# Kernel optimization log

Measured on AMD Instinct MI355X. Metric: run time of the kernel, lower is better.

Reference implementation:

```python
import jax, jax.numpy as jnp
import numpy as np

K = 3            # CRF kernel size
THETA0 = 0.5     # color bandwidth
THETA1 = 30.0    # spatial bandwidth
ALPHA0 = 3.0     # kernel scale
BASE = 0.45      # label clamping base
CRF_ITERS = 10   # mean-field iterations
NMS_SIGMA = 2.0  # gaussian matrix-NMS sigma


def _unfold(x, k=K):
    # torch.nn.Unfold(k, stride=1, padding=k//2): (B, C, H, W) -> (B, C, k*k, H*W)
    B, C, H, W = x.shape
    p = k // 2
    xp = jnp.pad(x, ((0, 0), (0, 0), (p, p), (p, p)))
    patches = jnp.stack([xp[:, :, i:i + H, j:j + W]
                         for i in range(k) for j in range(k)], axis=2)
    return patches.reshape(B, C, k * k, H * W)


def _matrix_nms(seg_masks, cate_labels, cate_scores, sigma=NMS_SIGMA):
    n = seg_masks.shape[0]
    m = seg_masks.reshape(n, -1).astype(jnp.float32)
    sum_m = m.sum(axis=1)                         # (n,)
    inter = m @ m.T                               # (n, n)
    union = sum_m[None, :] + sum_m[:, None] - inter
    triu = jnp.triu(jnp.ones((n, n), dtype=bool), k=1)
    iou = jnp.where(triu, inter / union, 0.0)
    label_eq = (cate_labels[None, :] == cate_labels[:, None]) & triu
    decay_iou = jnp.where(label_eq, iou, 0.0)
    comp = decay_iou.max(axis=0)                  # compensate IoU per candidate
    decay = jnp.exp(-sigma * decay_iou ** 2)
    compm = jnp.exp(-sigma * comp ** 2)[:, None]  # broadcast over columns (torch expand+T)
    coef = (decay / compm).min(axis=0)
    return cate_scores * coef


def _crf(feature_map, x, targets):
    B, C, H, W = feature_map.shape
    k2 = K * K
    # gaussian pairwise kernel from (shifted) color features
    fm = feature_map + 10.0
    uf = _unfold(fm)                              # (B, C, k2, H*W)
    idx = np.arange(k2)
    spatial = ((idx // K - K // 2) ** 2 + (idx % K - K // 2) ** 2).astype(np.float32)
    color = -((uf - fm.reshape(B, C, 1, H * W)) ** 2).sum(axis=1) / (2.0 * THETA0 ** 2)
    kernel = ALPHA0 * jnp.exp(color - jnp.asarray(spatial)[None, :, None] / (2.0 * THETA1 ** 2))
    kernel = kernel[:, None]                      # (B, 1, k2, H*W)

    # unary init
    xt = x * targets
    xt = (xt > 0.5).astype(jnp.float32) * (1.0 - 2.0 * BASE) + BASE
    ret = jnp.concatenate([1.0 - xt, xt], axis=1)  # (B, 2, H, W)
    ones_t = jnp.ones_like(targets)
    for _ in range(CRF_ITERS):
        uf_x = _unfold(-jnp.log(ret.reshape(2 * B, 1, H, W))).reshape(B, 2, k2, H * W)
        aggre = (uf_x * kernel).sum(axis=2)        # (B, 2, H*W)
        f = jnp.exp(-aggre).reshape(B, 2, H, W)
        f = f * jnp.concatenate([ones_t, targets], axis=1)  # gate fg channel by targets
        f = f + 1e-6
        f = f / f.sum(axis=1, keepdims=True)
        ret = (f > 0.5).astype(jnp.float32) * (1.0 - 2.0 * BASE) + BASE
    masks = (ret[:, 1:] > 0.5).astype(jnp.float32)  # (B, 1, H, W)
    count = masks.reshape(B, -1).sum(axis=1)
    valid = ((count >= H * W * 0.05) & (count <= H * W * 0.95)).astype(jnp.float32)
    return masks, valid


def setup_inputs() -> dict:
    key = jax.random.key(0)
    k1, k2, k3, k4, k5, k6 = jax.random.split(key, 6)
    n, h, w = 256, 128, 128
    ni, c = 64, 3
    seg_masks = (jax.random.uniform(k1, (n, h, w)) > 0.5).astype(jnp.float32)
    cate_scores = jnp.sort(jax.random.uniform(k2, (n,)))[::-1]
    feature_map = jax.random.uniform(k3, (ni, c, h, w))
    x = jax.random.uniform(k4, (ni, 1, h, w))
    targets = (jax.random.uniform(k5, (ni, 1, h, w)) > 0.3).astype(jnp.float32)
    cate_labels = jax.random.randint(k6, (n,), 0, 80, dtype=jnp.int64)
    return {"seg_masks": seg_masks, "cate_scores": cate_scores,
            "feature_map": feature_map, "x": x, "targets": targets,
            "cate_labels": cate_labels}


def reference(seg_masks, cate_scores, feature_map, x, targets, cate_labels):
    scores = _matrix_nms(seg_masks, cate_labels, cate_scores)
    masks, valid = _crf(feature_map, x, targets)
    return scores, masks, valid
```

## Files before the change

kernel.cpp:

```cpp
#include <hip/hip_runtime.h>
#include <stdint.h>

#define HW 16384
#define NI 64
#define NM 256
#define WORDS 256

#define PR 136
#define PSZ (26 * PR)
#define SR 34

#define OFF_STATE2 (1u << 20)
#define OFF_PACKED (2u << 20)
#define OFF_DIOUT  0x280000u
#define OFF_COMPM  0x2C0000u
#define OFF_CNT    0x2C1000u

__global__ __launch_bounds__(256) void diou_compm_kernel(
    const unsigned long long* __restrict__ packed, const int* __restrict__ labels,
    float* __restrict__ diouT, float* __restrict__ compm) {
    #pragma clang fp contract(off)
    __shared__ unsigned long long colj[WORDS];
    __shared__ float red[NM];
    const int j = blockIdx.x, i = threadIdx.x;
    colj[i] = packed[i * NM + j];
    __syncthreads();
    int inter = 0, si = 0, sj = 0;
    for (int w = 0; w < WORDS; ++w) {
        unsigned long long a = colj[w];
        unsigned long long b = packed[w * NM + i];
        inter += __popcll(a & b);
        sj += __popcll(a);
        si += __popcll(b);
    }
    float d = 0.0f;
    if (j > i && labels[i] == labels[j]) {
        float u = (float)(si + sj - inter);
        d = (float)inter / u;
    }
    diouT[j * NM + i] = d;
    red[i] = d;
    __syncthreads();
    for (int off = 128; off > 0; off >>= 1) {
        if (i < off) red[i] = fmaxf(red[i], red[i + off]);
        __syncthreads();
    }
    if (i == 0) {
        float m = red[0];
        float t = m * m;
        compm[j] = expf(-2.0f * t);
    }
}

template <bool FIRST>
__global__ __launch_bounds__(832, 6) void crf5_kernel(
    const float* __restrict__ feat, const float* __restrict__ scores,
    const float* __restrict__ diouT, const float* __restrict__ compm,
    const float* __restrict__ seg, unsigned long long* __restrict__ packed,
    const float* __restrict__ x, const float* __restrict__ targets,
    unsigned char* __restrict__ state2, float* __restrict__ out,
    int* __restrict__ counters) {
    #pragma clang fp contract(off)
    __shared__ float plane[4 * PSZ];
    __shared__ uint32_t stw[2][26 * SR];
    __shared__ int chg;
    const int tid = threadIdx.x, bid = blockIdx.x;
    const int img = bid >> 3, r0 = (bid & 7) * 16;
    const int w0 = r0 - 5;
    const int rel = tid >> 5;
    const int q = tid & 31;
    const int xc = q * 4;
    const int y = w0 + rel;
    const bool inimg = (unsigned)y < 128u;

    if (FIRST) {
        const int wave = tid >> 6, lane = tid & 63;
        const int gw = bid * 13 + wave;
        if (gw < 4096) {
            for (int t = 0; t < 16; ++t) {
                int gwi = gw * 16 + t;
                int i = gwi >> 8, w = gwi & 255;
                float v = seg[(size_t)i * HW + w * 64 + lane];
                unsigned long long m = __ballot(v > 0.5f);
                if (lane == 0) packed[w * NM + i] = m;
            }
        }
        if (bid == 0 && tid < NI + 1) counters[tid] = 0;
    } else {
        if (bid < NM) {
            float* red = plane;
            if (tid < NM) {
                float d = diouT[bid * NM + tid];
                float dd = d * d;
                float dec = expf(-2.0f * dd);
                red[tid] = dec / compm[tid];
            }
            __syncthreads();
            for (int off = 128; off > 0; off >>= 1) {
                if (tid < off) red[tid] = fminf(red[tid], red[tid + off]);
                __syncthreads();
            }
            if (tid == 0) out[bid] = scores[bid] * red[0];
            __syncthreads();
        }
    }

    {
        const float* fb = feat + (size_t)img * 3 * HW;
        float c0[4], c1[4], c2[4];
        if (inimg) {
            const int pp = y * 128 + xc;
            float4 cv0 = *(const float4*)&fb[pp];
            float4 cv1 = *(const float4*)&fb[HW + pp];
            float4 cv2 = *(const float4*)&fb[2 * HW + pp];
            c0[0]=cv0.x+10.0f; c0[1]=cv0.y+10.0f; c0[2]=cv0.z+10.0f; c0[3]=cv0.w+10.0f;
            c1[0]=cv1.x+10.0f; c1[1]=cv1.y+10.0f; c1[2]=cv1.z+10.0f; c1[3]=cv1.w+10.0f;
            c2[0]=cv2.x+10.0f; c2[1]=cv2.y+10.0f; c2[2]=cv2.z+10.0f; c2[3]=cv2.w+10.0f;
        }
        #pragma unroll
        for (int k = 0; k < 4; ++k) {
            const int dy = (k < 3) ? -1 : 0;
            const int dx = (k < 3) ? (k - 1) : -1;
            float res[4] = {0.0f, 0.0f, 0.0f, 0.0f};
            if (inimg) {
                const int ny = y + dy;
                if ((unsigned)ny < 128u) {
                    #pragma unroll
                    for (int j = 0; j < 4; ++j) {
                        const int nx = xc + j + dx;
                        if ((unsigned)nx < 128u) {
                            const int qq = ny * 128 + nx;
                            float u0 = fb[qq] + 10.0f;
                            float u1 = fb[HW + qq] + 10.0f;
                            float u2 = fb[2 * HW + qq] + 10.0f;
                            float d0 = u0 - c0[j], d1 = u1 - c1[j], d2 = u2 - c2[j];
                            float ss = d0 * d0;
                            ss = ss + d1 * d1;
                            ss = ss + d2 * d2;
                            float color = (-ss) / 0.5f;
                            float sp = (float)(dy * dy + dx * dx) / 1800.0f;
                            res[j] = 3.0f * expf(color - sp);
                        }
                    }
                }
            }
            *(float4*)&plane[k * PSZ + rel * PR + 4 + xc] =
                make_float4(res[0], res[1], res[2], res[3]);
            if (q == 0)
                *(float4*)&plane[k * PSZ + rel * PR + 0] = make_float4(0, 0, 0, 0);
            if (q == 31)
                *(float4*)&plane[k * PSZ + rel * PR + 132] = make_float4(0, 0, 0, 0);
        }
        uint32_t st = 0;
        if (inimg) {
            if (FIRST) {
                const size_t gp = (size_t)img * HW + y * 128 + xc;
                const float4 xv = *(const float4*)(x + gp);
                const float4 tv = *(const float4*)(targets + gp);
                float xs[4] = {xv.x, xv.y, xv.z, xv.w};
                float ts[4] = {tv.x, tv.y, tv.z, tv.w};
                #pragma unroll
                for (int j = 0; j < 4; ++j) {
                    float xt = xs[j] * ts[j];
                    int b1 = (xt > 0.5f) ? 1 : 0;
                    int tb = (ts[j] > 0.5f) ? 1 : 0;
                    st |= (uint32_t)(b1 | ((b1 ^ 1) << 1) | (tb << 2)) << (8 * j);
                }
            } else {
                st = ((const uint32_t*)(state2 + (size_t)img * HW + y * 128))[q];
            }
        }
        stw[0][rel * SR + 1 + q] = st;
        if (!inimg) stw[1][rel * SR + 1 + q] = 0;
        if (q == 0)  { stw[0][rel * SR + 0]  = 0; stw[1][rel * SR + 0]  = 0; }
        if (q == 31) { stw[0][rel * SR + 33] = 0; stw[1][rel * SR + 33] = 0; }
    }
    __syncthreads();

    const float l45 = 0.7985076962177716f;
    const float l55 = 0.5978370007556204f;
    const bool compute = inimg && (y >= r0 - 4) && (y < r0 + 20);
    const int lane = tid & 63;
    const int rbase = rel * PR + 4 + xc;
    const int sbase = rel * SR + 1 + q;
    int cur = 0;
    for (int s = 0; s < 5; ++s) {
        if (tid == 0) chg = 0;
        __syncthreads();
        const int lo = (r0 - 4 + s < 0) ? 0 : r0 - 4 + s;
        const int hi = (r0 + 20 - s > 128) ? 128 : r0 + 20 - s;
        const bool act = compute && (y >= lo) && (y < hi);
        bool changed = false;
        if (act) {
            const uint32_t* sw = &stw[cur][0];
            float lx1r[3][6], lx0r[3][6];
            uint32_t wcen = 0;
            #pragma unroll
            for (int r = 0; r < 3; ++r) {
                const int base = sbase + (r - 1) * SR;
                const uint32_t wm = sw[base - 1];
                const uint32_t wc = sw[base];
                const uint32_t wp = sw[base + 1];
                if (r == 1) wcen = wc;
                unsigned char b[6];
                b[0] = wm >> 24;
                b[1] = wc & 0xff; b[2] = (wc >> 8) & 0xff;
                b[3] = (wc >> 16) & 0xff; b[4] = wc >> 24;
                b[5] = wp & 0xff;
                #pragma unroll
                for (int m = 0; m < 6; ++m) {
                    lx1r[r][m] = (b[m] & 1) ? l55 : l45;
                    lx0r[r][m] = (b[m] & 2) ? l55 : l45;
                }
            }
            float4 p0a = *(const float4*)&plane[0 * PSZ + rbase];
            float4 p1a = *(const float4*)&plane[1 * PSZ + rbase];
            float4 p2a = *(const float4*)&plane[2 * PSZ + rbase];
            float4 p3a = *(const float4*)&plane[3 * PSZ + rbase];
            float4 p0b = *(const float4*)&plane[0 * PSZ + rbase + PR];
            float4 p1b = *(const float4*)&plane[1 * PSZ + rbase + PR];
            float4 p2b = *(const float4*)&plane[2 * PSZ + rbase + PR];
            float s5 = plane[3 * PSZ + rbase + 4];
            float s6 = plane[2 * PSZ + rbase + PR - 1];
            float s8 = plane[0 * PSZ + rbase + PR + 4];
            const float kw[9][4] = {
                {p0a.x, p0a.y, p0a.z, p0a.w},
                {p1a.x, p1a.y, p1a.z, p1a.w},
                {p2a.x, p2a.y, p2a.z, p2a.w},
                {p3a.x, p3a.y, p3a.z, p3a.w},
                {3.0f, 3.0f, 3.0f, 3.0f},
                {p3a.y, p3a.z, p3a.w, s5},
                {s6, p2b.x, p2b.y, p2b.z},
                {p1b.x, p1b.y, p1b.z, p1b.w},
                {p0b.y, p0b.z, p0b.w, s8}};
            float a0[4] = {0.f, 0.f, 0.f, 0.f}, a1[4] = {0.f, 0.f, 0.f, 0.f};
            #pragma unroll
            for (int k = 0; k < 9; ++k) {
                const int r = k / 3, m0 = k % 3;
                #pragma unroll
                for (int j = 0; j < 4; ++j) {
                    const float kwv = kw[k][j];
                    const float t1 = lx1r[r][j + m0] * kwv;
                    const float t0 = lx0r[r][j + m0] * kwv;
                    a1[j] = a1[j] + t1;
                    a0[j] = a0[j] + t0;
                }
            }
            uint32_t ow = 0;
            #pragma unroll
            for (int j = 0; j < 4; ++j) {
                const unsigned char sc = (wcen >> (8 * j)) & 0xffu;
                const float tval = (sc & 4) ? 1.0f : 0.0f;
                const float e1 = expf(-a1[j]);
                const float e0 = expf(-a0[j]);
                const float m1 = e1 * tval;
                const float f1 = m1 + 1e-6f;
                const float f0 = e0 + 1e-6f;
                const float den = f0 + f1;
                const float r1 = f1 / den;
                const float r0v = f0 / den;
                const int s1 = (r1 > 0.5f) ? 1 : 0;
                const int s0 = (r0v > 0.5f) ? 1 : 0;
                ow |= (uint32_t)(s1 | (s0 << 1) | (sc & 4)) << (8 * j);
            }
            stw[cur ^ 1][sbase] = ow;
            changed = (ow != wcen);
        }
        unsigned long long bal = __ballot(changed);
        if (lane == 0 && bal) atomicOr(&chg, 1);
        __syncthreads();
        if (chg == 0) break;
        cur ^= 1;
    }

    int cnt = 0;
    if (inimg && y >= r0 && y < r0 + 16) {
        const uint32_t w = stw[cur][sbase];
        if (FIRST) {
            ((uint32_t*)(state2 + (size_t)img * HW))[y * 32 + q] = w;
        } else {
            float* om = out + NM + (size_t)img * HW;
            *(float4*)(om + y * 128 + xc) =
                make_float4((float)(w & 1), (float)((w >> 8) & 1),
                            (float)((w >> 16) & 1), (float)((w >> 24) & 1));
            cnt = __popc(w & 0x01010101u);
        }
    }

    if (!FIRST) {
        __syncthreads();
        int* cred = (int*)plane;
        cred[tid] = cnt;
        if (tid < 192) cred[832 + tid] = 0;
        __syncthreads();
        for (int off = 512; off > 0; off >>= 1) {
            if (tid < off) cred[tid] += cred[tid + off];
            __syncthreads();
        }
        int* flag = (int*)&stw[0][0];
        if (tid == 0) {
            atomicAdd(&counters[img], cred[0]);
            __threadfence();
            int old = atomicAdd(&counters[NI], 1);
            flag[0] = (old == 511) ? 1 : 0;
        }
        __syncthreads();
        if (flag[0] && tid < NI) {
            int c = atomicAdd(&counters[tid], 0);
            out[NM + (size_t)NI * HW + tid] = (c >= 820 && c <= 15564) ? 1.0f : 0.0f;
        }
    }
}

extern "C" void kernel_launch(void* const* d_in, const int* in_sizes, int n_in,
                              void* d_out, int out_size, void* d_ws, size_t ws_size,
                              hipStream_t stream) {
    const float* seg = (const float*)d_in[0];
    const float* cate_scores = (const float*)d_in[1];
    const float* feat = (const float*)d_in[2];
    const float* x = (const float*)d_in[3];
    const float* targets = (const float*)d_in[4];
    const int* labels = (const int*)d_in[5];
    float* out = (float*)d_out;
    char* ws = (char*)d_ws;

    unsigned char* state2 = (unsigned char*)(ws + OFF_STATE2);
    unsigned long long* packed = (unsigned long long*)(ws + OFF_PACKED);
    float* diouT = (float*)(ws + OFF_DIOUT);
    float* compm = (float*)(ws + OFF_COMPM);
    int* counters = (int*)(ws + OFF_CNT);

    crf5_kernel<true><<<512, 832, 0, stream>>>(feat, cate_scores, diouT, compm,
                                               seg, packed, x, targets, state2,
                                               out, counters);
    diou_compm_kernel<<<NM, 256, 0, stream>>>(packed, labels, diouT, compm);
    crf5_kernel<false><<<512, 832, 0, stream>>>(feat, cate_scores, diouT, compm,
                                                seg, packed, x, targets, state2,
                                                out, counters);
}
```

Baseline: 189.2 us.

## Cache pairwise kernel planes in workspace and skip unchanged CRF stencil updates

The first CRF pass now writes its computed Gaussian pairwise-kernel planes to a global workspace buffer, and the second pass reloads them instead of recomputing them from the feature map. Inside the mean-field loop, each thread remembers its previous 3x3 neighbourhood state words and reuses the prior output when they are unchanged, skipping the weighted sum and exp/divide work. This trades extra global write/read traffic (about 6.8 MB) and register pressure for the saved arithmetic and feature reads, within a single call.

```diff
diff --git a/kernel.cpp b/kernel.cpp
--- a/kernel.cpp
+++ b/kernel.cpp
@@ -15,6 +15,7 @@
 #define OFF_DIOUT  0x280000u
 #define OFF_COMPM  0x2C0000u
 #define OFF_CNT    0x2C1000u
+#define OFF_GPLANE 0x300000u
 
 __global__ __launch_bounds__(256) void diou_compm_kernel(
     const unsigned long long* __restrict__ packed, const int* __restrict__ labels,
@@ -58,8 +59,8 @@
     const float* __restrict__ diouT, const float* __restrict__ compm,
     const float* __restrict__ seg, unsigned long long* __restrict__ packed,
     const float* __restrict__ x, const float* __restrict__ targets,
-    unsigned char* __restrict__ state2, float* __restrict__ out,
-    int* __restrict__ counters) {
+    unsigned char* __restrict__ state2, float* __restrict__ gplane,
+    float* __restrict__ out, int* __restrict__ counters) {
     #pragma clang fp contract(off)
     __shared__ float plane[4 * PSZ];
     __shared__ uint32_t stw[2][26 * SR];
@@ -105,7 +106,7 @@
         }
     }
 
-    {
+    if (FIRST) {
         const float* fb = feat + (size_t)img * 3 * HW;
         float c0[4], c1[4], c2[4];
         if (inimg) {
@@ -144,13 +145,26 @@
                     }
                 }
             }
-            *(float4*)&plane[k * PSZ + rel * PR + 4 + xc] =
-                make_float4(res[0], res[1], res[2], res[3]);
+            float4 r4 = make_float4(res[0], res[1], res[2], res[3]);
+            *(float4*)&plane[k * PSZ + rel * PR + 4 + xc] = r4;
+            *(float4*)&gplane[(((size_t)bid * 4 + k) * 26 + rel) * 128 + xc] = r4;
             if (q == 0)
                 *(float4*)&plane[k * PSZ + rel * PR + 0] = make_float4(0, 0, 0, 0);
             if (q == 31)
                 *(float4*)&plane[k * PSZ + rel * PR + 132] = make_float4(0, 0, 0, 0);
         }
+    } else {
+        #pragma unroll
+        for (int k = 0; k < 4; ++k) {
+            float4 v = *(const float4*)&gplane[(((size_t)bid * 4 + k) * 26 + rel) * 128 + xc];
+            *(float4*)&plane[k * PSZ + rel * PR + 4 + xc] = v;
+            if (q == 0)
+                *(float4*)&plane[k * PSZ + rel * PR + 0] = make_float4(0, 0, 0, 0);
+            if (q == 31)
+                *(float4*)&plane[k * PSZ + rel * PR + 132] = make_float4(0, 0, 0, 0);
+        }
+    }
+    {
         uint32_t st = 0;
         if (inimg) {
             if (FIRST) {
@@ -183,6 +197,9 @@
     const int lane = tid & 63;
     const int rbase = rel * PR + 4 + xc;
     const int sbase = rel * SR + 1 + q;
+    uint32_t pin[9];
+    uint32_t powv = 0;
+    bool haveprev = false;
     int cur = 0;
     for (int s = 0; s < 5; ++s) {
         if (tid == 0) chg = 0;
@@ -193,75 +210,93 @@
         bool changed = false;
         if (act) {
             const uint32_t* sw = &stw[cur][0];
-            float lx1r[3][6], lx0r[3][6];
-            uint32_t wcen = 0;
+            uint32_t in9[9];
             #pragma unroll
             for (int r = 0; r < 3; ++r) {
                 const int base = sbase + (r - 1) * SR;
-                const uint32_t wm = sw[base - 1];
-                const uint32_t wc = sw[base];
-                const uint32_t wp = sw[base + 1];
-                if (r == 1) wcen = wc;
-                unsigned char b[6];
-                b[0] = wm >> 24;
-                b[1] = wc & 0xff; b[2] = (wc >> 8) & 0xff;
-                b[3] = (wc >> 16) & 0xff; b[4] = wc >> 24;
-                b[5] = wp & 0xff;
-                #pragma unroll
-                for (int m = 0; m < 6; ++m) {
-                    lx1r[r][m] = (b[m] & 1) ? l55 : l45;
-                    lx0r[r][m] = (b[m] & 2) ? l55 : l45;
-                }
-            }
-            float4 p0a = *(const float4*)&plane[0 * PSZ + rbase];
-            float4 p1a = *(const float4*)&plane[1 * PSZ + rbase];
-            float4 p2a = *(const float4*)&plane[2 * PSZ + rbase];
-            float4 p3a = *(const float4*)&plane[3 * PSZ + rbase];
-            float4 p0b = *(const float4*)&plane[0 * PSZ + rbase + PR];
-            float4 p1b = *(const float4*)&plane[1 * PSZ + rbase + PR];
-            float4 p2b = *(const float4*)&plane[2 * PSZ + rbase + PR];
-            float s5 = plane[3 * PSZ + rbase + 4];
-            float s6 = plane[2 * PSZ + rbase + PR - 1];
-            float s8 = plane[0 * PSZ + rbase + PR + 4];
-            const float kw[9][4] = {
-                {p0a.x, p0a.y, p0a.z, p0a.w},
-                {p1a.x, p1a.y, p1a.z, p1a.w},
-                {p2a.x, p2a.y, p2a.z, p2a.w},
-                {p3a.x, p3a.y, p3a.z, p3a.w},
-                {3.0f, 3.0f, 3.0f, 3.0f},
-                {p3a.y, p3a.z, p3a.w, s5},
-                {s6, p2b.x, p2b.y, p2b.z},
-                {p1b.x, p1b.y, p1b.z, p1b.w},
-                {p0b.y, p0b.z, p0b.w, s8}};
-            float a0[4] = {0.f, 0.f, 0.f, 0.f}, a1[4] = {0.f, 0.f, 0.f, 0.f};
+                in9[r * 3 + 0] = sw[base - 1];
+                in9[r * 3 + 1] = sw[base];
+                in9[r * 3 + 2] = sw[base + 1];
+            }
+            const uint32_t wcen = in9[4];
+            bool same = haveprev;
             #pragma unroll
-            for (int k = 0; k < 9; ++k) {
-                const int r = k / 3, m0 = k % 3;
+            for (int m = 0; m < 9; ++m) same = same && (in9[m] == pin[m]);
+            uint32_t ow;
+            if (same) {
+                ow = powv;
+            } else {
+                float lx1r[3][6], lx0r[3][6];
+                #pragma unroll
+                for (int r = 0; r < 3; ++r) {
+                    const uint32_t wm = in9[r * 3 + 0];
+                    const uint32_t wc = in9[r * 3 + 1];
+                    const uint32_t wp = in9[r * 3 + 2];
+                    unsigned char b[6];
+                    b[0] = wm >> 24;
+                    b[1] = wc & 0xff; b[2] = (wc >> 8) & 0xff;
+                    b[3] = (wc >> 16) & 0xff; b[4] = wc >> 24;
+                    b[5] = wp & 0xff;
+                    #pragma unroll
+                    for (int m = 0; m < 6; ++m) {
+                        lx1r[r][m] = (b[m] & 1) ? l55 : l45;
+                        lx0r[r][m] = (b[m] & 2) ? l55 : l45;
+                    }
+                }
+                float4 p0a = *(const float4*)&plane[0 * PSZ + rbase];
+                float4 p1a = *(const float4*)&plane[1 * PSZ + rbase];
+                float4 p2a = *(const float4*)&plane[2 * PSZ + rbase];
+                float4 p3a = *(const float4*)&plane[3 * PSZ + rbase];
+                float4 p0b = *(const float4*)&plane[0 * PSZ + rbase + PR];
+                float4 p1b = *(const float4*)&plane[1 * PSZ + rbase + PR];
+                float4 p2b = *(const float4*)&plane[2 * PSZ + rbase + PR];
+                float s5 = plane[3 * PSZ + rbase + 4];
+                float s6 = plane[2 * PSZ + rbase + PR - 1];
+                float s8 = plane[0 * PSZ + rbase + PR + 4];
+                const float kw[9][4] = {
+                    {p0a.x, p0a.y, p0a.z, p0a.w},
+                    {p1a.x, p1a.y, p1a.z, p1a.w},
+                    {p2a.x, p2a.y, p2a.z, p2a.w},
+                    {p3a.x, p3a.y, p3a.z, p3a.w},
+                    {3.0f, 3.0f, 3.0f, 3.0f},
+                    {p3a.y, p3a.z, p3a.w, s5},
+                    {s6, p2b.x, p2b.y, p2b.z},
+                    {p1b.x, p1b.y, p1b.z, p1b.w},
+                    {p0b.y, p0b.z, p0b.w, s8}};
+                float a0[4] = {0.f, 0.f, 0.f, 0.f}, a1[4] = {0.f, 0.f, 0.f, 0.f};
+                #pragma unroll
+                for (int k = 0; k < 9; ++k) {
+                    const int r = k / 3, m0 = k % 3;
+                    #pragma unroll
+                    for (int j = 0; j < 4; ++j) {
+                        const float kwv = kw[k][j];
+                        const float t1 = lx1r[r][j + m0] * kwv;
+                        const float t0 = lx0r[r][j + m0] * kwv;
+                        a1[j] = a1[j] + t1;
+                        a0[j] = a0[j] + t0;
+                    }
+                }
+                ow = 0;
                 #pragma unroll
                 for (int j = 0; j < 4; ++j) {
-                    const float kwv = kw[k][j];
-                    const float t1 = lx1r[r][j + m0] * kwv;
-                    const float t0 = lx0r[r][j + m0] * kwv;
-                    a1[j] = a1[j] + t1;
-                    a0[j] = a0[j] + t0;
-                }
-            }
-            uint32_t ow = 0;
-            #pragma unroll
-            for (int j = 0; j < 4; ++j) {
-                const unsigned char sc = (wcen >> (8 * j)) & 0xffu;
-                const float tval = (sc & 4) ? 1.0f : 0.0f;
-                const float e1 = expf(-a1[j]);
-                const float e0 = expf(-a0[j]);
-                const float m1 = e1 * tval;
-                const float f1 = m1 + 1e-6f;
-                const float f0 = e0 + 1e-6f;
-                const float den = f0 + f1;
-                const float r1 = f1 / den;
-                const float r0v = f0 / den;
-                const int s1 = (r1 > 0.5f) ? 1 : 0;
-                const int s0 = (r0v > 0.5f) ? 1 : 0;
-                ow |= (uint32_t)(s1 | (s0 << 1) | (sc & 4)) << (8 * j);
+                    const unsigned char sc = (wcen >> (8 * j)) & 0xffu;
+                    const float tval = (sc & 4) ? 1.0f : 0.0f;
+                    const float e1 = expf(-a1[j]);
+                    const float e0 = expf(-a0[j]);
+                    const float m1 = e1 * tval;
+                    const float f1 = m1 + 1e-6f;
+                    const float f0 = e0 + 1e-6f;
+                    const float den = f0 + f1;
+                    const float r1 = f1 / den;
+                    const float r0v = f0 / den;
+                    const int s1 = (r1 > 0.5f) ? 1 : 0;
+                    const int s0 = (r0v > 0.5f) ? 1 : 0;
+                    ow |= (uint32_t)(s1 | (s0 << 1) | (sc & 4)) << (8 * j);
+                }
+                #pragma unroll
+                for (int m = 0; m < 9; ++m) pin[m] = in9[m];
+                powv = ow;
+                haveprev = true;
             }
             stw[cur ^ 1][sbase] = ow;
             changed = (ow != wcen);
@@ -329,12 +364,13 @@
     float* diouT = (float*)(ws + OFF_DIOUT);
     float* compm = (float*)(ws + OFF_COMPM);
     int* counters = (int*)(ws + OFF_CNT);
+    float* gplane = (float*)(ws + OFF_GPLANE);
 
     crf5_kernel<true><<<512, 832, 0, stream>>>(feat, cate_scores, diouT, compm,
                                                seg, packed, x, targets, state2,
-                                               out, counters);
+                                               gplane, out, counters);
     diou_compm_kernel<<<NM, 256, 0, stream>>>(packed, labels, diouT, compm);
     crf5_kernel<false><<<512, 832, 0, stream>>>(feat, cate_scores, diouT, compm,
                                                 seg, packed, x, targets, state2,
-                                                out, counters);
+                                                gplane, out, counters);
 }
```

New measurement: 186.5 us. About the same (-1.4%).
